# Kernel tuning notes

Hardware: AMD Instinct MI355X
Metric: run time of the kernel (lower is better)

Reference implementation:

```python
import jax, jax.numpy as jnp
import numpy as np

K = 3
OH = 62
OW = 62


def setup_inputs() -> dict:
    key = jax.random.key(0)
    k1, k2 = jax.random.split(key)
    x = jax.random.normal(k1, (32, 32, 64, 64), dtype=jnp.float32)
    W = jax.random.normal(k2, (64, 32, OH, OW, K, K), dtype=jnp.float32)
    b = jnp.zeros((64, OH, OW), dtype=jnp.float32)
    return {"x": x, "W": W, "b": b}


def _patches(x):
    # x: [B, C, H, W] -> [B, C, OH, OW, K, K] (stride-1 unfold, small K*K loop)
    return jnp.stack(
        [jnp.stack([x[:, :, i:i + OH, j:j + OW] for j in range(K)], axis=-1)
         for i in range(K)], axis=-2)


def reference(x, W, b):
    # Locally connected: per-location independent weights.
    # out[b,o,h,w] = sum_{c,i,j} x[b,c,h+i,w+j] * W[o,c,h,w,i,j] + b[o,h,w]
    p = _patches(x)  # [B, C, OH, OW, K, K]
    out = jnp.einsum('bchwij,ochwij->bohw', p, W) + b[None]
    return out
```

## Files before the change

kernel.cpp:

```cpp
#include <hip/hip_runtime.h>


#define C_  32
#define B_  32
#define O_  64
#define H_  64
#define W_  64
#define OH_ 62
#define OW_ 62

typedef float vfloat2 __attribute__((ext_vector_type(2)));
typedef float vfloat4 __attribute__((ext_vector_type(4)));

#define GLL4(gaddr, laddr)                                                      \
    __builtin_amdgcn_global_load_lds(                                           \
        (const __attribute__((address_space(1))) void*)(gaddr),                 \
        (__attribute__((address_space(3))) void*)(laddr), 4, 0, 0)

__device__ __forceinline__ float dpp_nextlane(float v) {
    return __int_as_float(__builtin_amdgcn_update_dpp(
        0, __float_as_int(v), 0x101, 0xf, 0xf, true));
}

#define WAITV(n) do {                                                           \
        asm volatile("s_waitcnt vmcnt(" #n ")" ::: "memory");                   \
        __builtin_amdgcn_sched_barrier(0);                                      \
    } while (0)

__global__ __launch_bounds__(256)
void lcl_kernel(const float* __restrict__ x,
                const float* __restrict__ Wt,
                const float* __restrict__ bias,
                float* __restrict__ out) {
    __shared__ float ldsW[2][4][2][576];

    const int i0      = blockIdx.x;
    const int logical = (i0 & 7) * 62 + (i0 >> 3);
    const int og      = logical & 7;
    const int h       = logical >> 3;

    const int wv_i = threadIdx.x >> 6;
    const int o0   = (og << 3) + (wv_i << 1);
    const int lane = threadIdx.x & 63;
    const int wg   = lane & 15;
    const int bg   = lane >> 4;
    const int w0   = wg * 4;
    const int b0   = bg * 8;
    const bool full = (wg < 15);

    float acc0[8][4], acc1[8][4];
#pragma unroll
    for (int bi = 0; bi < 8; ++bi)
#pragma unroll
        for (int wi = 0; wi < 4; ++wi) { acc0[bi][wi] = 0.f; acc1[bi][wi] = 0.f; }

    const long wrow0 = (long)o0 * (C_ * 34596) + (long)h * 558;
    const long wrow1 = wrow0 + (long)C_ * 34596;

    const char* xb0 = (const char*)x + (unsigned)b0 * 524288u
                      + (unsigned)h * 256u + (unsigned)wg * 16u;

#define STAGE_W2(buf, cidx) do {                                                \
        const char* s0_ = (const char*)(Wt + wrow0 + (long)(cidx) * 34596);     \
        const char* s1_ = (const char*)(Wt + wrow1 + (long)(cidx) * 34596);     \
        char* d0_ = (char*)&ldsW[buf][wv_i][0][0];                              \
        char* d1_ = (char*)&ldsW[buf][wv_i][1][0];                              \
        _Pragma("unroll")                                                       \
        for (int k_ = 0; k_ < 8; ++k_)                                          \
            GLL4(s0_ + k_ * 256 + lane * 4, d0_ + k_ * 256);                    \
        GLL4(s0_ + 1976 + lane * 4, d0_ + 1976);                                \
        _Pragma("unroll")                                                       \
        for (int k_ = 0; k_ < 8; ++k_)                                          \
            GLL4(s1_ + k_ * 256 + lane * 4, d1_ + k_ * 256);                    \
        GLL4(s1_ + 1976 + lane * 4, d1_ + 1976);                                \
    } while (0)

#define DSREAD_W2(buf) do {                                                     \
        const char* r0_ = (const char*)&ldsW[buf][wv_i][0][0] + wg * 144;       \
        const char* r1_ = (const char*)&ldsW[buf][wv_i][1][0] + wg * 144;       \
        _Pragma("unroll")                                                       \
        for (int q_ = 0; q_ < 9; ++q_) {                                        \
            wq0[q_] = *reinterpret_cast<const vfloat4*>(r0_ + q_ * 16);         \
            wq1[q_] = *reinterpret_cast<const vfloat4*>(r1_ + q_ * 16);         \
        }                                                                       \
    } while (0)

#define WQ0(t) (wq0[(t) >> 2][(t) & 3])
#define WQ1(t) (wq1[(t) >> 2][(t) & 3])

#define XLD(s_, cidx, bi_) do {                                                 \
        const char* p_ = xb0 + (unsigned)(bi_) * 524288u                        \
                         + (unsigned)(cidx) * 16384u;                           \
        xv##s_[0] = *reinterpret_cast<const float4*>(p_);                       \
        xv##s_[1] = *reinterpret_cast<const float4*>(p_ + 256);                 \
        xv##s_[2] = *reinterpret_cast<const float4*>(p_ + 512);                 \
    } while (0)

#define FMA2(s_, bi_) do {                                                      \
        float xr_[3][6];                                                        \
        _Pragma("unroll")                                                       \
        for (int r_ = 0; r_ < 3; ++r_) {                                        \
            xr_[r_][0] = xv##s_[r_].x; xr_[r_][1] = xv##s_[r_].y;               \
            xr_[r_][2] = xv##s_[r_].z; xr_[r_][3] = xv##s_[r_].w;               \
            xr_[r_][4] = dpp_nextlane(xv##s_[r_].x);                            \
            xr_[r_][5] = dpp_nextlane(xv##s_[r_].y);                            \
        }                                                                       \
        _Pragma("unroll")                                                       \
        for (int wi_ = 0; wi_ < 4; ++wi_)                                       \
        _Pragma("unroll")                                                       \
        for (int ii_ = 0; ii_ < 3; ++ii_)                                       \
        _Pragma("unroll")                                                       \
        for (int j_ = 0; j_ < 3; ++j_) {                                        \
            acc0[bi_][wi_] = fmaf(xr_[ii_][wi_ + j_],                           \
                                  WQ0(wi_ * 9 + ii_ * 3 + j_), acc0[bi_][wi_]); \
            acc1[bi_][wi_] = fmaf(xr_[ii_][wi_ + j_],                           \
                                  WQ1(wi_ * 9 + ii_ * 3 + j_), acc1[bi_][wi_]); \
        }                                                                       \
    } while (0)

    vfloat4 wq0[9], wq1[9];
    float4  xvA[3], xvB[3], xvC[3];

    STAGE_W2(0, 0);
    STAGE_W2(1, 1);

    for (int c = 0; c < C_; ++c) {
        WAITV(18);
        DSREAD_W2(c & 1);
        XLD(A, c, 0);
        XLD(B, c, 1);
        __builtin_amdgcn_sched_barrier(0);
        XLD(C, c, 2); FMA2(A, 0);
        XLD(A, c, 3); FMA2(B, 1);
        XLD(B, c, 4); FMA2(C, 2);
        XLD(C, c, 5); FMA2(A, 3);
        XLD(A, c, 6); FMA2(B, 4);
        XLD(B, c, 7); FMA2(C, 5);
        __builtin_amdgcn_sched_barrier(0);
        {
            const int cn = (c + 2 < C_) ? (c + 2) : (C_ - 1);
            STAGE_W2((c + 2) & 1, cn);
        }
        __builtin_amdgcn_sched_barrier(0);
        FMA2(A, 6);
        FMA2(B, 7);
    }

#pragma unroll
    for (int oo = 0; oo < 2; ++oo) {
        const int oc = o0 + oo;
        const float* brow = bias + ((long)oc * OH_ + h) * OW_ + w0;
        float2 bv0 = *reinterpret_cast<const float2*>(brow);
        float2 bv1;
        if (full) bv1 = *reinterpret_cast<const float2*>(brow + 2);
        else { bv1.x = 0.f; bv1.y = 0.f; }
#pragma unroll
        for (int bi = 0; bi < 8; ++bi) {
            const float* a_ = oo ? acc1[bi] : acc0[bi];
            float* orow = out + (((long)(b0 + bi) * O_ + oc) * OH_ + h) * OW_ + w0;
            vfloat2 s0; s0.x = a_[0] + bv0.x; s0.y = a_[1] + bv0.y;
            __builtin_nontemporal_store(s0, reinterpret_cast<vfloat2*>(orow));
            if (full) {
                vfloat2 s1; s1.x = a_[2] + bv1.x; s1.y = a_[3] + bv1.y;
                __builtin_nontemporal_store(s1, reinterpret_cast<vfloat2*>(orow) + 1);
            }
        }
    }

#undef STAGE_W2
#undef DSREAD_W2
#undef WQ0
#undef WQ1
#undef XLD
#undef FMA2
}

extern "C" void kernel_launch(void* const* d_in, const int* in_sizes, int n_in,
                              void* d_out, int out_size, void* d_ws, size_t ws_size,
                              hipStream_t stream) {
    const float* x    = (const float*)d_in[0];
    const float* Wt   = (const float*)d_in[1];
    const float* bias = (const float*)d_in[2];
    float* out        = (float*)d_out;

    dim3 grid(8 * OH_);
    dim3 block(256);
    lcl_kernel<<<grid, block, 0, stream>>>(x, Wt, bias, out);
}
```

Measured before the change: 157.7 us.

## Split batch across paired blocks and process output channels sequentially

Doubles the grid so each block handles half the batch (16 images instead of 32), and interleaves the two batch halves across the block index so paired blocks share the same weight slice and likely the same L2. Inside the channel loop the two output channels are now handled one after the other, reusing a single weight-register array, and four x slices are loaded up front. This cuts accumulator and weight register pressure to raise occupancy and latency hiding. The cost is that the weight tensor, which dominates memory traffic, is fetched twice unless the second fetch hits in cache.

```diff
diff --git a/kernel.cpp b/kernel.cpp
--- a/kernel.cpp
+++ b/kernel.cpp
@@ -27,6 +27,8 @@
         __builtin_amdgcn_sched_barrier(0);                                      \
     } while (0)
 
+#define FENCE() __builtin_amdgcn_sched_barrier(0)
+
 __global__ __launch_bounds__(256)
 void lcl_kernel(const float* __restrict__ x,
                 const float* __restrict__ Wt,
@@ -35,9 +37,11 @@
     __shared__ float ldsW[2][4][2][576];
 
     const int i0      = blockIdx.x;
-    const int logical = (i0 & 7) * 62 + (i0 >> 3);
-    const int og      = logical & 7;
-    const int h       = logical >> 3;
+    const int logical = (i0 & 7) * 124 + (i0 >> 3);
+    const int bhalf   = logical & 1;
+    const int pair    = logical >> 1;
+    const int og      = pair & 7;
+    const int h       = pair >> 3;
 
     const int wv_i = threadIdx.x >> 6;
     const int o0   = (og << 3) + (wv_i << 1);
@@ -45,12 +49,12 @@
     const int wg   = lane & 15;
     const int bg   = lane >> 4;
     const int w0   = wg * 4;
-    const int b0   = bg * 8;
+    const int b0   = bhalf * 16 + bg * 4;
     const bool full = (wg < 15);
 
-    float acc0[8][4], acc1[8][4];
+    float acc0[4][4], acc1[4][4];
 #pragma unroll
-    for (int bi = 0; bi < 8; ++bi)
+    for (int bi = 0; bi < 4; ++bi)
 #pragma unroll
         for (int wi = 0; wi < 4; ++wi) { acc0[bi][wi] = 0.f; acc1[bi][wi] = 0.f; }
 
@@ -75,18 +79,14 @@
         GLL4(s1_ + 1976 + lane * 4, d1_ + 1976);                                \
     } while (0)
 
-#define DSREAD_W2(buf) do {                                                     \
-        const char* r0_ = (const char*)&ldsW[buf][wv_i][0][0] + wg * 144;       \
-        const char* r1_ = (const char*)&ldsW[buf][wv_i][1][0] + wg * 144;       \
+#define DSREAD_W(buf, oo_) do {                                                 \
+        const char* r_ = (const char*)&ldsW[buf][wv_i][oo_][0] + wg * 144;      \
         _Pragma("unroll")                                                       \
-        for (int q_ = 0; q_ < 9; ++q_) {                                        \
-            wq0[q_] = *reinterpret_cast<const vfloat4*>(r0_ + q_ * 16);         \
-            wq1[q_] = *reinterpret_cast<const vfloat4*>(r1_ + q_ * 16);         \
-        }                                                                       \
+        for (int q_ = 0; q_ < 9; ++q_)                                          \
+            wq[q_] = *reinterpret_cast<const vfloat4*>(r_ + q_ * 16);           \
     } while (0)
 
-#define WQ0(t) (wq0[(t) >> 2][(t) & 3])
-#define WQ1(t) (wq1[(t) >> 2][(t) & 3])
+#define WQ(t) (wq[(t) >> 2][(t) & 3])
 
 #define XLD(s_, cidx, bi_) do {                                                 \
         const char* p_ = xb0 + (unsigned)(bi_) * 524288u                        \
@@ -96,7 +96,7 @@
         xv##s_[2] = *reinterpret_cast<const float4*>(p_ + 512);                 \
     } while (0)
 
-#define FMA2(s_, bi_) do {                                                      \
+#define FMA1(ACC, s_, bi_) do {                                                 \
         float xr_[3][6];                                                        \
         _Pragma("unroll")                                                       \
         for (int r_ = 0; r_ < 3; ++r_) {                                        \
@@ -110,40 +110,42 @@
         _Pragma("unroll")                                                       \
         for (int ii_ = 0; ii_ < 3; ++ii_)                                       \
         _Pragma("unroll")                                                       \
-        for (int j_ = 0; j_ < 3; ++j_) {                                        \
-            acc0[bi_][wi_] = fmaf(xr_[ii_][wi_ + j_],                           \
-                                  WQ0(wi_ * 9 + ii_ * 3 + j_), acc0[bi_][wi_]); \
-            acc1[bi_][wi_] = fmaf(xr_[ii_][wi_ + j_],                           \
-                                  WQ1(wi_ * 9 + ii_ * 3 + j_), acc1[bi_][wi_]); \
-        }                                                                       \
+        for (int j_ = 0; j_ < 3; ++j_)                                          \
+            ACC[bi_][wi_] = fmaf(xr_[ii_][wi_ + j_],                            \
+                                 WQ(wi_ * 9 + ii_ * 3 + j_), ACC[bi_][wi_]);    \
     } while (0)
 
-    vfloat4 wq0[9], wq1[9];
-    float4  xvA[3], xvB[3], xvC[3];
+    vfloat4 wq[9];
+    float4  xvA[3], xvB[3], xvC[3], xvD[3];
 
     STAGE_W2(0, 0);
     STAGE_W2(1, 1);
 
     for (int c = 0; c < C_; ++c) {
+        const int p = c & 1;
         WAITV(18);
-        DSREAD_W2(c & 1);
+        DSREAD_W(p, 0);
         XLD(A, c, 0);
         XLD(B, c, 1);
-        __builtin_amdgcn_sched_barrier(0);
-        XLD(C, c, 2); FMA2(A, 0);
-        XLD(A, c, 3); FMA2(B, 1);
-        XLD(B, c, 4); FMA2(C, 2);
-        XLD(C, c, 5); FMA2(A, 3);
-        XLD(A, c, 6); FMA2(B, 4);
-        XLD(B, c, 7); FMA2(C, 5);
-        __builtin_amdgcn_sched_barrier(0);
+        XLD(C, c, 2);
+        XLD(D, c, 3);
+        FENCE();
+        FMA1(acc0, A, 0);
+        FMA1(acc0, B, 1);
+        FMA1(acc0, C, 2);
+        FMA1(acc0, D, 3);
+        FENCE();
+        DSREAD_W(p, 1);
+        FENCE();
+        FMA1(acc1, A, 0);
+        FMA1(acc1, B, 1);
+        FMA1(acc1, C, 2);
+        FMA1(acc1, D, 3);
+        FENCE();
         {
             const int cn = (c + 2 < C_) ? (c + 2) : (C_ - 1);
-            STAGE_W2((c + 2) & 1, cn);
+            STAGE_W2(p, cn);
         }
-        __builtin_amdgcn_sched_barrier(0);
-        FMA2(A, 6);
-        FMA2(B, 7);
     }
 
 #pragma unroll
@@ -155,7 +157,7 @@
         if (full) bv1 = *reinterpret_cast<const float2*>(brow + 2);
         else { bv1.x = 0.f; bv1.y = 0.f; }
 #pragma unroll
-        for (int bi = 0; bi < 8; ++bi) {
+        for (int bi = 0; bi < 4; ++bi) {
             const float* a_ = oo ? acc1[bi] : acc0[bi];
             float* orow = out + (((long)(b0 + bi) * O_ + oc) * OH_ + h) * OW_ + w0;
             vfloat2 s0; s0.x = a_[0] + bv0.x; s0.y = a_[1] + bv0.y;
@@ -168,11 +170,10 @@
     }
 
 #undef STAGE_W2
-#undef DSREAD_W2
-#undef WQ0
-#undef WQ1
+#undef DSREAD_W
+#undef WQ
 #undef XLD
-#undef FMA2
+#undef FMA1
 }
 
 extern "C" void kernel_launch(void* const* d_in, const int* in_sizes, int n_in,
@@ -183,7 +184,7 @@
     const float* bias = (const float*)d_in[2];
     float* out        = (float*)d_out;
 
-    dim3 grid(8 * OH_);
+    dim3 grid(992);
     dim3 block(256);
     lcl_kernel<<<grid, block, 0, stream>>>(x, Wt, bias, out);
 }
```

After: 140.1 us. 11.2% less time.
